# Kernel optimization log

Hardware: AMD Instinct MI355X
Metric: run time of the kernel (lower is better)

The kernel has to match this reference:

```python
import jax, jax.numpy as jnp
import numpy as np

# ---- column/activation layout (matches transformer_info init kwarg) ----
N_COLS = 20          # continuous data columns
MODES = 50           # VGM modes per column (gumbel-softmax width)
SPAN = MODES + 1     # 1 tanh scalar + MODES gumbel logits
IN_DIM = 2048
OUT_DIM = N_COLS * SPAN  # 1020
TAU = 0.2
B = 16384
EPS = 1e-9

_spans = []
for i in range(N_COLS):
    st = i * SPAN
    _spans.append((st, st + 1, 0))          # tanh span (alpha)
    _spans.append((st + 1, st + SPAN, 1))   # gumbel-softmax span (beta/d)
N_SEG = len(_spans)

_seg = np.zeros(OUT_DIM, np.int32)   # segment id per output feature
_typ = np.zeros(OUT_DIM, np.int32)   # 0 = tanh, 1 = gumbel-softmax
for si, (s, e, t) in enumerate(_spans):
    _seg[s:e] = si
    _typ[s:e] = t
SEG = jnp.asarray(_seg)
TYP = jnp.asarray(_typ)


def setup_inputs() -> dict:
    key = jax.random.key(0)
    kx, kw, kb, ku = jax.random.split(key, 4)
    bound = 1.0 / np.sqrt(IN_DIM)  # init_bounded(dim=input_dim)
    x = jax.random.normal(kx, (B, IN_DIM), dtype=jnp.float32)
    W = jax.random.uniform(kw, (IN_DIM, OUT_DIM), minval=-bound, maxval=bound, dtype=jnp.float32)
    b = jax.random.uniform(kb, (OUT_DIM,), minval=-bound, maxval=bound, dtype=jnp.float32)
    u = jax.random.uniform(ku, (B, OUT_DIM), dtype=jnp.float32)  # uniform driving gumbel noise
    return {"x": x, "W": W, "b": b, "u": u}


def _segment_softmax(z):
    # softmax over each transformer_info span, fused via segment ops.
    zT = z.T  # [D, B]
    m = jax.ops.segment_max(zT, SEG, num_segments=N_SEG)      # [S, B]
    e = jnp.exp(zT - m[SEG])
    s = jax.ops.segment_sum(e, SEG, num_segments=N_SEG)       # [S, B]
    return (e / s[SEG]).T  # [B, D]


def reference(x, W, b, u):
    outputs = x @ W + b  # [B, OUT_DIM]
    # Gumbel(0,1) noise from uniform u
    g = -jnp.log(-jnp.log(jnp.clip(u, EPS, 1.0 - EPS)))
    soft = _segment_softmax((outputs + g) / TAU)
    # type 0 -> tanh, type 1 -> gumbel-softmax (single fused select)
    data_t = jnp.where(TYP == 0, jnp.tanh(outputs), soft)
    return outputs, data_t
```

## Files before the change

### kernel.cpp

```cpp
#include <hip/hip_runtime.h>
#include <stdint.h>

#define MDIM 16384
#define NDIM 1020
#define KDIM 2048
#define NPAD 1024
#define TK   (KDIM / 64)

typedef __attribute__((ext_vector_type(4))) float f32x4;
typedef __attribute__((ext_vector_type(8))) short short8;

#define MFMA16(a, b, c) __builtin_amdgcn_mfma_f32_16x16x32_bf16((a), (b), (c), 0, 0, 0)

template <int OFF>
static __device__ __forceinline__ short8 dsr(unsigned addr) {
    short8 r;
    asm volatile("ds_read_b128 %0, %1 offset:%2" : "=v"(r) : "v"(addr), "i"(OFF));
    return r;
}
template <int OFF>
static __device__ __forceinline__ void dsw64(unsigned addr, uint2 v) {
    asm volatile("ds_write_b64 %0, %1 offset:%2" :: "v"(addr), "v"(v), "i"(OFF));
}

__device__ __forceinline__ unsigned packbf(float lo, float hi) {
    const unsigned r0 = __float_as_uint(lo) + 0x8000u;
    const unsigned r1 = __float_as_uint(hi) + 0x8000u;
    return __builtin_amdgcn_perm(r1, r0, 0x07060302u);
}

__device__ __forceinline__ unsigned short f2bf(float f) {
    unsigned int u = __float_as_uint(f);
    unsigned int r = (u + 0x7FFFu + ((u >> 16) & 1u)) >> 16;
    return (unsigned short)r;
}

__global__ void prep_w_kernel(const float* __restrict__ W,
                              unsigned short* __restrict__ Wt) {
    const int id = blockIdx.x * 256 + threadIdx.x;
    const int n0 = (id & 255) * 4;
    const int k0 = (id >> 8) * 4;
    float a[4][4];
    if (n0 < NDIM) {
#pragma unroll
        for (int i = 0; i < 4; ++i) {
            const float* p = W + (size_t)(k0 + i) * NDIM + n0;
            a[i][0] = p[0]; a[i][1] = p[1]; a[i][2] = p[2]; a[i][3] = p[3];
        }
    } else {
#pragma unroll
        for (int i = 0; i < 4; ++i)
#pragma unroll
            for (int j = 0; j < 4; ++j) a[i][j] = 0.f;
    }
#pragma unroll
    for (int j = 0; j < 4; ++j) {
        uint2 p;
        p.x = (unsigned)f2bf(a[0][j]) | ((unsigned)f2bf(a[1][j]) << 16);
        p.y = (unsigned)f2bf(a[2][j]) | ((unsigned)f2bf(a[3][j]) << 16);
        *(uint2*)(Wt + (size_t)(n0 + j) * KDIM + k0) = p;
    }
}

__global__ void prep_x_kernel(const float* __restrict__ x,
                              unsigned short* __restrict__ Xb) {
    const size_t total = (size_t)MDIM * KDIM;
    const size_t stride = (size_t)gridDim.x * 256 * 8;
    for (size_t i = ((size_t)blockIdx.x * 256 + threadIdx.x) * 8; i < total; i += stride) {
        const float4 v0 = *(const float4*)(x + i);
        const float4 v1 = *(const float4*)(x + i + 4);
        uint4 p;
        p.x = (unsigned)f2bf(v0.x) | ((unsigned)f2bf(v0.y) << 16);
        p.y = (unsigned)f2bf(v0.z) | ((unsigned)f2bf(v0.w) << 16);
        p.z = (unsigned)f2bf(v1.x) | ((unsigned)f2bf(v1.y) << 16);
        p.w = (unsigned)f2bf(v1.z) | ((unsigned)f2bf(v1.w) << 16);
        *(uint4*)(Xb + i) = p;
    }
}

extern "C" __global__ __launch_bounds__(512, 1) void gemm11_kernel(
    const float* __restrict__ x,
    const unsigned short* __restrict__ Wt,
    const float* __restrict__ bias,
    float* __restrict__ out) {
    extern __shared__ unsigned short lds_raw[];

    const int tid  = threadIdx.x;
    const int lane = tid & 63;
    const int wid  = tid >> 6;
    const int wr   = wid >> 2;
    const int wc   = wid & 3;

    const int bid = blockIdx.x;
    const int swz = (bid & 7) * 32 + (bid >> 3);
    const int bm  = swz >> 2;
    const int bn  = swz & 3;

    const int srow = wid * 8 + (lane >> 3);
    const int scb  = ((lane & 7) ^ (lane >> 3)) * 8;
    const unsigned short* bS = Wt + (size_t)(bn * 256 + srow) * KDIM + scb;

#define STAGEB(BUFI, STRIPE, S) do {                                             \
    const unsigned short* sp_ =                                                  \
        bS + (size_t)((STRIPE) * 64) * KDIM + (size_t)(((S) & 31) * 64);         \
    __builtin_amdgcn_global_load_lds(                                            \
        (const __attribute__((address_space(1))) unsigned int*)sp_,              \
        (__attribute__((address_space(3))) unsigned int*)(lds_raw +              \
            (BUFI) * 32768 + 16384 + ((STRIPE) * 64 + wid * 8) * 64),            \
        16, 0, 0);                                                               \
} while (0)

    const int h = lane >> 4, g = lane & 15;
    const float* aF = x + (size_t)(bm * 256 + wid * 32 + h) * KDIM + g * 4;

    const unsigned ldsbase =
        (unsigned)(uintptr_t)(__attribute__((address_space(3))) unsigned short*)lds_raw;
    const unsigned awbE =
        ldsbase + (unsigned)(wid * 32 + h) * 128 +
        ((unsigned)((g >> 1) ^ h) << 4) + (unsigned)(g & 1) * 8;
    const unsigned awbO  = awbE ^ 0x40u;
    const unsigned awb0E = awbE,           awb0O = awbO;
    const unsigned awb1E = awbE + 65536u,  awb1O = awbO + 65536u;

    float4 av[8];
#define AGLD(T) {                                                     \
    const float* ap_ = aF + (size_t)(((T) & 31) * 64);                \
    av[0] = *(const float4*)(ap_);                                    \
    av[1] = *(const float4*)(ap_ + 4 * KDIM);                         \
    av[2] = *(const float4*)(ap_ + 8 * KDIM);                         \
    av[3] = *(const float4*)(ap_ + 12 * KDIM);                        \
    av[4] = *(const float4*)(ap_ + 16 * KDIM);                        \
    av[5] = *(const float4*)(ap_ + 20 * KDIM);                        \
    av[6] = *(const float4*)(ap_ + 24 * KDIM);                        \
    av[7] = *(const float4*)(ap_ + 28 * KDIM);                        \
}
#define CVT1(AWE, AWO, I)                                             \
    { uint2 v_;                                                       \
      v_.x = packbf(av[I].x, av[I].y);                                \
      v_.y = packbf(av[I].z, av[I].w);                                \
      dsw64<(I) * 512>(((I) & 1) ? (AWO) : (AWE), v_); }
#define CVTW(AWE, AWO)                                                \
    CVT1(AWE, AWO, 0) CVT1(AWE, AWO, 1) CVT1(AWE, AWO, 2)             \
    CVT1(AWE, AWO, 3) CVT1(AWE, AWO, 4) CVT1(AWE, AWO, 5)             \
    CVT1(AWE, AWO, 6) CVT1(AWE, AWO, 7)

    const unsigned l15 = lane & 15, hi = lane >> 4, l7 = lane & 7;
    const unsigned c0 = (unsigned)((0 * 4 + hi) ^ l7) << 4;
    const unsigned c1 = (unsigned)((1 * 4 + hi) ^ l7) << 4;
    const unsigned pbA = ldsbase + (unsigned)(wr * 128 + l15) * 128;
    const unsigned pbB = ldsbase + 32768u + (unsigned)(wc * 64 + l15) * 128;
    const unsigned aA0_0 = pbA + c0,          aA0_1 = pbA + c1;
    const unsigned aA1_0 = pbA + 65536u + c0, aA1_1 = pbA + 65536u + c1;
    const unsigned bB0_0 = pbB + c0,          bB0_1 = pbB + c1;
    const unsigned bB1_0 = pbB + 65536u + c0, bB1_1 = pbB + 65536u + c1;

    f32x4 acc[8][4];
#pragma unroll
    for (int i = 0; i < 8; ++i)
#pragma unroll
        for (int j = 0; j < 4; ++j) {
            f32x4 z = {0.f, 0.f, 0.f, 0.f};
            acc[i][j] = z;
        }

#define PH_TAIL                                                       \
    __builtin_amdgcn_s_barrier();                                     \
    asm volatile("s_waitcnt lgkmcnt(0)" ::: "memory");                \
    __builtin_amdgcn_sched_barrier(0);                                \
    __builtin_amdgcn_s_setprio(1);

#define PH_MFMA(MF0)                                                  \
    _Pragma("unroll")                                                 \
    for (int k2 = 0; k2 < 2; ++k2)                                    \
        _Pragma("unroll")                                             \
        for (int nf = 0; nf < 4; ++nf) {                              \
            acc[MF0][nf]     = MFMA16(af0[k2], bfv[nf][k2], acc[MF0][nf]);     \
            acc[MF0 + 1][nf] = MFMA16(af1[k2], bfv[nf][k2], acc[MF0 + 1][nf]); \
        }                                                             \
    __builtin_amdgcn_s_setprio(0);

#define RDA(BUF, MF0)                                                 \
    af0[0] = dsr<(MF0) * 2048>(aA##BUF##_0);                          \
    af0[1] = dsr<(MF0) * 2048>(aA##BUF##_1);                          \
    af1[0] = dsr<(MF0) * 2048 + 2048>(aA##BUF##_0);                   \
    af1[1] = dsr<(MF0) * 2048 + 2048>(aA##BUF##_1);

#define RDB(BUF, NF)                                                  \
    bfv[NF][0] = dsr<(NF) * 2048>(bB##BUF##_0);                       \
    bfv[NF][1] = dsr<(NF) * 2048>(bB##BUF##_1);

#define TILE(T, BUF, NB, AWE, AWO)                                              \
  {                                                                             \
    short8 bfv[4][2];                                                           \
    short8 af0[2], af1[2];                                                      \
           \
    RDB(BUF, 0) RDB(BUF, 1) RDB(BUF, 2) RDB(BUF, 3)                             \
    RDA(BUF, 0)                                                                 \
    AGLD((T) + 1)                                                               \
    PH_TAIL                                                                     \
    PH_MFMA(0)                                                                  \
    __builtin_amdgcn_s_barrier();                                               \
                         \
    RDA(BUF, 2)                                                                 \
    STAGEB(BUF, 0, (T) + 2); STAGEB(BUF, 1, (T) + 2);                           \
    PH_TAIL                                                                     \
    PH_MFMA(2)                                                                  \
    __builtin_amdgcn_s_barrier();                                               \
                        \
    RDA(BUF, 4)                                                                 \
    STAGEB(BUF, 2, (T) + 2); STAGEB(BUF, 3, (T) + 2);                           \
    PH_TAIL                                                                     \
    PH_MFMA(4)                                                                  \
    __builtin_amdgcn_s_barrier();                                               \
              \
    RDA(BUF, 6)                                                                 \
    CVTW(AWE, AWO)                                                              \
    PH_TAIL                                                                     \
    PH_MFMA(6)                                                                  \
    __builtin_amdgcn_s_barrier();                                               \
  }

    AGLD(0)
    STAGEB(0, 0, 0); STAGEB(0, 1, 0); STAGEB(0, 2, 0); STAGEB(0, 3, 0);
    CVTW(awb0E, awb0O)
    STAGEB(1, 0, 1); STAGEB(1, 1, 1); STAGEB(1, 2, 1); STAGEB(1, 3, 1);
    asm volatile("s_waitcnt vmcnt(4)" ::: "memory");
    __builtin_amdgcn_sched_barrier(0);
    asm volatile("s_waitcnt lgkmcnt(0)" ::: "memory");
    __builtin_amdgcn_sched_barrier(0);
    __builtin_amdgcn_s_barrier();

    for (int t2 = 0; t2 < TK; t2 += 2) {
        TILE(t2,     0, 1, awb1E, awb1O)
        TILE(t2 + 1, 1, 0, awb0E, awb0O)
    }

#pragma unroll
    for (int nf = 0; nf < 4; ++nf) {
        const int col = bn * 256 + wc * 64 + nf * 16 + (lane & 15);
        if (col < NDIM) {
            const float bv = bias[col];
#pragma unroll
            for (int mf = 0; mf < 8; ++mf) {
                const int row = bm * 256 + wr * 128 + mf * 16 + ((lane >> 4) << 2);
                float* op = out + (size_t)row * NDIM + col;
#pragma unroll
                for (int r = 0; r < 4; ++r)
                    op[(size_t)r * NDIM] = acc[mf][nf][r] + bv;
            }
        }
    }
#undef STAGEB
#undef AGLD
#undef CVT1
#undef CVTW
#undef PH_TAIL
#undef PH_MFMA
#undef RDA
#undef RDB
#undef TILE
}

__global__ void gemm_bf_kernel(const unsigned short* __restrict__ Xb,
                               const unsigned short* __restrict__ Wt,
                               const float* __restrict__ bias,
                               float* __restrict__ out) {
    __shared__ __align__(16) unsigned short As[128][32];
    __shared__ __align__(16) unsigned short Bs[128][32];

    const int tid  = threadIdx.x;
    const int lane = tid & 63;
    const int wid  = tid >> 6;
    const int wr   = wid >> 1;
    const int wc   = wid & 1;
    const int bn   = blockIdx.x;
    const int bm   = blockIdx.y;

    f32x4 acc[4][4];
#pragma unroll
    for (int i = 0; i < 4; ++i)
#pragma unroll
        for (int j = 0; j < 4; ++j) {
            f32x4 z = {0.f, 0.f, 0.f, 0.f};
            acc[i][j] = z;
        }

    const unsigned short* abase =
        Xb + (size_t)(bm * 128 + wid * 16 + (lane >> 2)) * KDIM + (lane & 3) * 8;
    const unsigned short* bbase =
        Wt + (size_t)(bn * 128 + wid * 16 + (lane >> 2)) * KDIM + (lane & 3) * 8;

    for (int kt = 0; kt < KDIM; kt += 32) {
#pragma unroll
        for (int j = 0; j < 2; ++j)
            __builtin_amdgcn_global_load_lds(
                (const __attribute__((address_space(1))) unsigned int*)(abase + (size_t)j * 64 * KDIM + kt),
                (__attribute__((address_space(3))) unsigned int*)(&As[j * 64 + wid * 16][0]),
                16, 0, 0);
#pragma unroll
        for (int j = 0; j < 2; ++j)
            __builtin_amdgcn_global_load_lds(
                (const __attribute__((address_space(1))) unsigned int*)(bbase + (size_t)j * 64 * KDIM + kt),
                (__attribute__((address_space(3))) unsigned int*)(&Bs[j * 64 + wid * 16][0]),
                16, 0, 0);
        __syncthreads();

        short8 af[4], bfr[4];
#pragma unroll
        for (int mi = 0; mi < 4; ++mi)
            af[mi] = *(const short8*)&As[wr * 64 + mi * 16 + (lane & 15)][(lane >> 4) * 8];
#pragma unroll
        for (int ni = 0; ni < 4; ++ni)
            bfr[ni] = *(const short8*)&Bs[wc * 64 + ni * 16 + (lane & 15)][(lane >> 4) * 8];

#pragma unroll
        for (int mi = 0; mi < 4; ++mi)
#pragma unroll
            for (int ni = 0; ni < 4; ++ni)
                acc[mi][ni] = MFMA16(af[mi], bfr[ni], acc[mi][ni]);

        __syncthreads();
    }

#pragma unroll
    for (int ni = 0; ni < 4; ++ni) {
        const int col = bn * 128 + wc * 64 + ni * 16 + (lane & 15);
        if (col < NDIM) {
            const float bv = bias[col];
#pragma unroll
            for (int mi = 0; mi < 4; ++mi) {
                const int row = bm * 128 + wr * 64 + mi * 16 + ((lane >> 4) << 2);
                float* op = out + (size_t)row * NDIM + col;
#pragma unroll
                for (int r = 0; r < 4; ++r)
                    op[(size_t)r * NDIM] = acc[mi][ni][r] + bv;
            }
        }
    }
}

__global__ void act_kernel(const float* __restrict__ outp,
                           const float* __restrict__ u,
                           float* __restrict__ dt) {
    const int lane  = threadIdx.x & 63;
    const int gwave = (blockIdx.x * 256 + threadIdx.x) >> 6;
    const int nwave = gridDim.x * 4;
    const int total = MDIM * 20;
    const float NEG_INF = -__builtin_inff();

    for (int unit = gwave; unit < total; unit += nwave) {
        const int row = unit / 20;
        const int sp  = unit - row * 20;
        const size_t base = (size_t)row * NDIM + sp * 51;

        float o = 0.f, uu = 0.5f;
        if (lane < 51) {
            o  = outp[base + lane];
            uu = u[base + lane];
        }
        const bool soft = (lane >= 1) && (lane < 51);

        const float uc = fmaxf(uu, 1e-9f);
        const float g  = -__logf(-__logf(uc));
        float z = soft ? (o + g) * 5.0f : NEG_INF;

        float m = z;
#pragma unroll
        for (int off = 32; off; off >>= 1) m = fmaxf(m, __shfl_xor(m, off));
        float e = soft ? __expf(z - m) : 0.f;
        float s = e;
#pragma unroll
        for (int off = 32; off; off >>= 1) s += __shfl_xor(s, off);

        float res;
        if (lane == 0) {
            const float ex = __expf(-2.0f * fabsf(o));
            const float t  = (1.0f - ex) / (1.0f + ex);
            res = copysignf(t, o);
        } else {
            res = e / s;
        }
        if (lane < 51) dt[base + lane] = res;
    }
}

extern "C" void kernel_launch(void* const* d_in, const int* in_sizes, int n_in,
                              void* d_out, int out_size, void* d_ws, size_t ws_size,
                              hipStream_t stream) {
    const float* x = (const float*)d_in[0];
    const float* W = (const float*)d_in[1];
    const float* b = (const float*)d_in[2];
    const float* u = (const float*)d_in[3];
    float* out = (float*)d_out;
    float* dt  = out + (size_t)MDIM * NDIM;
    unsigned short* Wt = (unsigned short*)d_ws;
    unsigned short* Xb = Wt + (size_t)NPAD * KDIM;

    prep_w_kernel<<<512, 256, 0, stream>>>(W, Wt);

    const hipError_t attr_ok = hipFuncSetAttribute(
        (const void*)gemm11_kernel, hipFuncAttributeMaxDynamicSharedMemorySize, 131072);
    if (attr_ok == hipSuccess) {
        gemm11_kernel<<<256, 512, 131072, stream>>>(x, Wt, b, out);
    } else {
        prep_x_kernel<<<2048, 256, 0, stream>>>(x, Xb);
        gemm_bf_kernel<<<dim3(8, 128), 256, 0, stream>>>(Xb, Wt, b, out);
    }

    act_kernel<<<8192, 256, 0, stream>>>(out, u, dt);
}
```

Before: 184.7 us.

## Fuse tanh/gumbel-softmax epilogue into GEMM with span-aligned column tiles

Changes the N tiling so each block covers 255 columns (5 whole spans), which lets the activation run inside the GEMM epilogue. The accumulator tile is staged through LDS and each wave computes the per-span softmax and tanh with wave shuffles, writing data_t directly. This removes the separate act_kernel launch and its re-read of the outputs matrix. In exchange it adds a serialized epilogue, extra barriers, and overlapping redundant W tile columns.

```diff
diff --git a/kernel.cpp b/kernel.cpp
--- a/kernel.cpp
+++ b/kernel.cpp
@@ -78,11 +78,13 @@
     }
 }
 
-extern "C" __global__ __launch_bounds__(512, 1) void gemm11_kernel(
+extern "C" __global__ __launch_bounds__(512, 1) void gemm12_kernel(
     const float* __restrict__ x,
     const unsigned short* __restrict__ Wt,
     const float* __restrict__ bias,
-    float* __restrict__ out) {
+    const float* __restrict__ u,
+    float* __restrict__ out,
+    float* __restrict__ dt) {
     extern __shared__ unsigned short lds_raw[];
 
     const int tid  = threadIdx.x;
@@ -96,9 +98,9 @@
     const int bm  = swz >> 2;
     const int bn  = swz & 3;
 
-    const int srow = wid * 8 + (lane >> 3);
+    const int srow = bn * 255 + wid * 8 + (lane >> 3);
     const int scb  = ((lane & 7) ^ (lane >> 3)) * 8;
-    const unsigned short* bS = Wt + (size_t)(bn * 256 + srow) * KDIM + scb;
+    const unsigned short* bS = Wt + (size_t)srow * KDIM + scb;
 
 #define STAGEB(BUFI, STRIPE, S) do {                                             \
     const unsigned short* sp_ =                                                  \
@@ -193,26 +195,26 @@
   {                                                                             \
     short8 bfv[4][2];                                                           \
     short8 af0[2], af1[2];                                                      \
-           \
+                          \
     RDB(BUF, 0) RDB(BUF, 1) RDB(BUF, 2) RDB(BUF, 3)                             \
     RDA(BUF, 0)                                                                 \
     AGLD((T) + 1)                                                               \
     PH_TAIL                                                                     \
     PH_MFMA(0)                                                                  \
     __builtin_amdgcn_s_barrier();                                               \
-                         \
+                                        \
     RDA(BUF, 2)                                                                 \
     STAGEB(BUF, 0, (T) + 2); STAGEB(BUF, 1, (T) + 2);                           \
     PH_TAIL                                                                     \
     PH_MFMA(2)                                                                  \
     __builtin_amdgcn_s_barrier();                                               \
-                        \
+                                       \
     RDA(BUF, 4)                                                                 \
     STAGEB(BUF, 2, (T) + 2); STAGEB(BUF, 3, (T) + 2);                           \
     PH_TAIL                                                                     \
     PH_MFMA(4)                                                                  \
     __builtin_amdgcn_s_barrier();                                               \
-              \
+                     \
     RDA(BUF, 6)                                                                 \
     CVTW(AWE, AWO)                                                              \
     PH_TAIL                                                                     \
@@ -235,20 +237,86 @@
         TILE(t2 + 1, 1, 0, awb0E, awb0O)
     }
 
+    asm volatile("s_waitcnt vmcnt(0) lgkmcnt(0)" ::: "memory");
+    __builtin_amdgcn_sched_barrier(0);
+    __syncthreads();
+
+    float bv[4];
 #pragma unroll
     for (int nf = 0; nf < 4; ++nf) {
-        const int col = bn * 256 + wc * 64 + nf * 16 + (lane & 15);
+        int col = bn * 255 + wc * 64 + nf * 16 + (int)l15;
+        bv[nf] = bias[col < NDIM ? col : NDIM - 1];
+    }
+
+#pragma unroll
+    for (int nf = 0; nf < 4; ++nf) {
+        const int col = bn * 255 + wc * 64 + nf * 16 + (int)l15;
         if (col < NDIM) {
-            const float bv = bias[col];
 #pragma unroll
             for (int mf = 0; mf < 8; ++mf) {
                 const int row = bm * 256 + wr * 128 + mf * 16 + ((lane >> 4) << 2);
                 float* op = out + (size_t)row * NDIM + col;
 #pragma unroll
                 for (int r = 0; r < 4; ++r)
-                    op[(size_t)r * NDIM] = acc[mf][nf][r] + bv;
+                    op[(size_t)r * NDIM] = acc[mf][nf][r] + bv[nf];
             }
         }
+    }
+
+    float* lf = (float*)lds_raw;
+    const float NEG_INF = -__builtin_inff();
+
+#pragma unroll 1
+    for (int hh = 0; hh < 2; ++hh) {
+        if (wr == hh) {
+#pragma unroll
+            for (int mf = 0; mf < 8; ++mf)
+#pragma unroll
+                for (int nf = 0; nf < 4; ++nf)
+#pragma unroll
+                    for (int r = 0; r < 4; ++r) {
+                        const int rloc = mf * 16 + (int)hi * 4 + r;
+                        lf[rloc * 256 + wc * 64 + nf * 16 + (int)l15] =
+                            acc[mf][nf][r] + bv[nf];
+                    }
+        }
+        __syncthreads();
+
+#pragma unroll 1
+        for (int rl = 0; rl < 16; ++rl) {
+            const int rloc = wid * 16 + rl;
+            const int rowg = bm * 256 + hh * 128 + rloc;
+#pragma unroll
+            for (int sp = 0; sp < 5; ++sp) {
+                const int cl = sp * 51 + lane;
+                float o = 0.f, uu = 0.5f;
+                if (lane < 51) {
+                    o  = lf[rloc * 256 + cl];
+                    uu = u[(size_t)rowg * NDIM + bn * 255 + cl];
+                }
+                const bool soft = (lane >= 1) && (lane < 51);
+                const float uc = fmaxf(uu, 1e-9f);
+                const float gg = -__logf(-__logf(uc));
+                float z = soft ? (o + gg) * 5.0f : NEG_INF;
+                float m = z;
+#pragma unroll
+                for (int off = 32; off; off >>= 1) m = fmaxf(m, __shfl_xor(m, off));
+                float e = soft ? __expf(z - m) : 0.f;
+                float s = e;
+#pragma unroll
+                for (int off = 32; off; off >>= 1) s += __shfl_xor(s, off);
+                float res;
+                if (lane == 0) {
+                    const float ex = __expf(-2.0f * fabsf(o));
+                    const float t  = (1.0f - ex) / (1.0f + ex);
+                    res = copysignf(t, o);
+                } else {
+                    res = e / s;
+                }
+                if (lane < 51) dt[(size_t)rowg * NDIM + bn * 255 + cl] = res;
+            }
+        }
+        __syncthreads();
     }
 #undef STAGEB
 #undef AGLD
@@ -399,13 +467,12 @@
     prep_w_kernel<<<512, 256, 0, stream>>>(W, Wt);
 
     const hipError_t attr_ok = hipFuncSetAttribute(
-        (const void*)gemm11_kernel, hipFuncAttributeMaxDynamicSharedMemorySize, 131072);
+        (const void*)gemm12_kernel, hipFuncAttributeMaxDynamicSharedMemorySize, 131072);
     if (attr_ok == hipSuccess) {
-        gemm11_kernel<<<256, 512, 131072, stream>>>(x, Wt, b, out);
+        gemm12_kernel<<<256, 512, 131072, stream>>>(x, Wt, b, u, out, dt);
     } else {
         prep_x_kernel<<<2048, 256, 0, stream>>>(x, Xb);
         gemm_bf_kernel<<<dim3(8, 128), 256, 0, stream>>>(Xb, Wt, b, out);
-    }
-
-    act_kernel<<<8192, 256, 0, stream>>>(out, u, dt);
-}
+        act_kernel<<<8192, 256, 0, stream>>>(out, u, dt);
+    }
+}
```

After: 275.4 us. +49.1%, slower.
